# Kernel optimization log

Hardware: AMD Instinct MI355X
Metric: run time of the kernel (lower is better)

## Reference

```python
import jax, jax.numpy as jnp
import numpy as np

N, M, K, KD = 400000, 300000, 27, 8
CIN, C0, NCLS = 4, 32, 19
EPS = 1e-5


def setup_inputs() -> dict:
    key = jax.random.key(0)
    ks = jax.random.split(key, 20)
    point_fea = jax.random.normal(ks[0], (N, CIN), jnp.float32)
    idx_query = jax.random.randint(ks[1], (N,), 0, M, jnp.int32)
    nbrs = jax.random.randint(ks[2], (M, K), -1, M, jnp.int32)  # -1 = missing neighbor
    idx_dev = jax.random.randint(ks[3], (N, KD), -1, M, jnp.int32)
    w_raw = jax.random.uniform(ks[4], (N, KD), jnp.float32)
    w_dev = w_raw / jnp.sum(w_raw, axis=1, keepdims=True)  # trilinear weights sum to 1
    def w(k, *shape):
        fan = shape[-2] * K if len(shape) == 3 else shape[0]
        return jax.random.normal(k, shape, jnp.float32) / np.sqrt(fan)
    return {
        'point_fea': point_fea, 'idx_query': idx_query, 'nbrs': nbrs,
        'idx_dev': idx_dev, 'w_dev': w_dev,
        'W_s1': w(ks[5], K, CIN, C0), 'W_s2': w(ks[6], K, C0, C0),
        'g_s1': jnp.ones((C0,)), 'b_s1': jnp.zeros((C0,)),
        'g_s2': jnp.ones((C0,)), 'b_s2': jnp.zeros((C0,)),
        'W_r1': w(ks[7], K, C0, C0), 'W_r2': w(ks[8], K, C0, C0),
        'g_r1': jnp.ones((C0,)), 'b_r1': jnp.zeros((C0,)),
        'g_r2': jnp.ones((C0,)), 'b_r2': jnp.zeros((C0,)),
        'W_c': w(ks[9], C0, NCLS), 'b_c': jnp.zeros((NCLS,)),
    }


def sparse_conv(x, W, nbrs):
    # x: [M, Cin], W: [K, Cin, Cout], nbrs: [M, K] (-1 = miss)
    out = jnp.zeros((x.shape[0], W.shape[2]), x.dtype)
    for k in range(W.shape[0]):  # fixed small kernel-offset loop
        idx = nbrs[:, k]
        g = jnp.where((idx >= 0)[:, None], x[jnp.clip(idx, 0)], 0.0)
        out = out + g @ W[k]
    return out


def bn(x, g, b):
    m = jnp.mean(x, axis=0)
    v = jnp.var(x, axis=0)
    return (x - m) * jax.lax.rsqrt(v + EPS) * g + b


def reference(point_fea, idx_query, nbrs, idx_dev, w_dev,
              W_s1, W_s2, g_s1, b_s1, g_s2, b_s2,
              W_r1, W_r2, g_r1, b_r1, g_r2, b_r2, W_c, b_c):
    # spvoxelize: per-voxel mean of point features
    counts = jax.ops.segment_sum(jnp.ones((N,), jnp.float32), idx_query, M)
    vox = jax.ops.segment_sum(point_fea, idx_query, M) / jnp.maximum(counts, 1.0)[:, None]
    # stem: two sparse 3x3x3 convs + BN + ReLU
    h = jax.nn.relu(bn(sparse_conv(vox, W_s1, nbrs), g_s1, b_s1))
    h = jax.nn.relu(bn(sparse_conv(h, W_s2, nbrs), g_s2, b_s2))
    # ResidualBlock (inc == outc, stride 1 -> identity downsample)
    r = jax.nn.relu(bn(sparse_conv(h, W_r1, nbrs), g_r1, b_r1))
    r = bn(sparse_conv(r, W_r2, nbrs), g_r2, b_r2)
    h = jax.nn.relu(r + h)
    # spdevoxelize: masked trilinear 8-neighbor gather back to points
    g = jnp.where((idx_dev >= 0)[:, :, None], h[jnp.clip(idx_dev, 0)], 0.0)  # [N,8,C]
    pts = jnp.einsum('nkc,nk->nc', g, w_dev)
    # classifier
    return pts @ W_c + b_c
```

## Files before the change

kernel.cpp:

```cpp
#include <hip/hip_runtime.h>
#include <hip/hip_fp16.h>

#define NPTS 400000
#define MVOX 300000
#define KK 27
#define KD 8
#define CIN 4
#define C0 32
#define NCLS 19
#define EPS 1e-5f
#define NTILE (MVOX / 16)
#define GS1 ((MVOX + 255) / 256)
#define GT ((NTILE + 3) / 4)
#define NRED 64

typedef __attribute__((ext_vector_type(8))) _Float16 half8;
typedef __attribute__((ext_vector_type(4))) float f32x4;

__device__ __forceinline__ uint32_t pack2(float a, float b) {
    __half2 h = __floats2half2_rn(a, b);
    return __builtin_bit_cast(uint32_t, h);
}
__device__ __forceinline__ float2 unpack2(uint32_t u) {
    return __half22float2(__builtin_bit_cast(__half2, u));
}
__device__ __forceinline__ void unpack8(uint4 u, float* f) {
    float2 a = unpack2(u.x), b = unpack2(u.y), c = unpack2(u.z), d = unpack2(u.w);
    f[0] = a.x; f[1] = a.y; f[2] = b.x; f[3] = b.y;
    f[4] = c.x; f[5] = c.y; f[6] = d.x; f[7] = d.y;
}
__device__ __forceinline__ uint4 pack8(const float* f) {
    return make_uint4(pack2(f[0], f[1]), pack2(f[2], f[3]),
                      pack2(f[4], f[5]), pack2(f[6], f[7]));
}

__global__ void vox_accum(const float* __restrict__ pf, const int* __restrict__ iq,
                          float* __restrict__ counts, float* __restrict__ vox) {
    int i = blockIdx.x * blockDim.x + threadIdx.x;
    if (i >= NPTS) return;
    int q = iq[i];
    float4 f = *reinterpret_cast<const float4*>(pf + (size_t)i * CIN);
    atomicAdd(&counts[q], 1.0f);
    atomicAdd(&vox[q * CIN + 0], f.x);
    atomicAdd(&vox[q * CIN + 1], f.y);
    atomicAdd(&vox[q * CIN + 2], f.z);
    atomicAdd(&vox[q * CIN + 3], f.w);
}

__global__ void vox_div_h(const float4* __restrict__ vox, const float* __restrict__ counts,
                          uint2* __restrict__ voxh) {
    int i = blockIdx.x * blockDim.x + threadIdx.x;
    if (i >= MVOX) return;
    float inv = 1.0f / fmaxf(counts[i], 1.0f);
    float4 v = vox[i];
    voxh[i] = make_uint2(pack2(v.x * inv, v.y * inv), pack2(v.z * inv, v.w * inv));
}

__global__ void wprep(const float* __restrict__ W0, const float* __restrict__ W1,
                      const float* __restrict__ W2, uint4* __restrict__ Wf) {
    int t = blockIdx.x * blockDim.x + threadIdx.x;
    if (t >= 3 * KK * 128) return;
    int layer = t / (KK * 128);
    int rem = t % (KK * 128);
    int k = rem / 128;
    int h = (rem >> 6) & 1;
    int lane = rem & 63;
    const float* W = (layer == 0) ? W0 : (layer == 1) ? W1 : W2;
    const float* wk = W + k * (C0 * C0);
    int co = h * 16 + (lane & 15);
    int ci0 = (lane >> 4) * 8;
    float f[8];
#pragma unroll
    for (int j = 0; j < 8; j++) f[j] = wk[(ci0 + j) * C0 + co];
    Wf[t] = pack8(f);
}

__global__ __launch_bounds__(256) void conv_s1_h(const uint2* __restrict__ x,
                                                 const int* __restrict__ nbrs,
                                                 const float* __restrict__ W,
                                                 uint4* __restrict__ out,
                                                 float* __restrict__ partials) {
    int i = blockIdx.x * blockDim.x + threadIdx.x;
    const bool active = i < MVOX;
    float acc[C0];
#pragma unroll
    for (int c = 0; c < C0; c++) acc[c] = 0.f;
    if (active) {
        const int* nb = nbrs + (size_t)i * KK;
        int nbv[KK];
#pragma unroll
        for (int k = 0; k < KK; k++) nbv[k] = nb[k];
        uint2 pf[4];
#pragma unroll
        for (int k = 0; k < 4; k++) pf[k] = x[nbv[k] < 0 ? 0 : nbv[k]];
#pragma unroll
        for (int k = 0; k < KK; k++) {
            uint2 r = pf[k & 3];
            if (k + 4 < KK) pf[k & 3] = x[nbv[k + 4] < 0 ? 0 : nbv[k + 4]];
            float m = (nbv[k] >= 0) ? 1.f : 0.f;
            float2 ab = unpack2(r.x), cd = unpack2(r.y);
            float xs[4] = {m * ab.x, m * ab.y, m * cd.x, m * cd.y};
            const float* wk = W + k * (CIN * C0);
#pragma unroll
            for (int j = 0; j < 4; j++) {
#pragma unroll
                for (int co = 0; co < C0; co++) acc[co] += xs[j] * wk[j * C0 + co];
            }
        }
        uint4* o = out + (size_t)i * 4;
#pragma unroll
        for (int p = 0; p < 4; p++) o[p] = pack8(acc + p * 8);
    }
    float q[C0];
#pragma unroll
    for (int c = 0; c < C0; c++) q[c] = acc[c] * acc[c];
#pragma unroll
    for (int off = 32; off >= 1; off >>= 1) {
#pragma unroll
        for (int c = 0; c < C0; c++) {
            acc[c] += __shfl_down(acc[c], off);
            q[c] += __shfl_down(q[c], off);
        }
    }
    __shared__ float ls[4][64];
    const int wid = threadIdx.x >> 6, lane = threadIdx.x & 63;
    if (lane == 0) {
#pragma unroll
        for (int c = 0; c < C0; c++) { ls[wid][c] = acc[c]; ls[wid][C0 + c] = q[c]; }
    }
    __syncthreads();
    if (threadIdx.x < 64)
        partials[(size_t)blockIdx.x * 64 + threadIdx.x] =
            ls[0][threadIdx.x] + ls[1][threadIdx.x] + ls[2][threadIdx.x] + ls[3][threadIdx.x];
}

__global__ __launch_bounds__(256, 4) void conv32_mfma(const uint4* __restrict__ x,
                                                      const int* __restrict__ nbrs,
                                                      const uint4* __restrict__ Wf,
                                                      const float* __restrict__ ss,
                                                      __half* __restrict__ out,
                                                      float* __restrict__ partials) {
    const int lane = threadIdx.x & 63;
    const int wid = threadIdx.x >> 6;
    const int tile = blockIdx.x * 4 + wid;
    const bool active = tile < NTILE;
    const int row = lane & 15;
    const int chunk = lane >> 4;
    const int col = lane & 15;
    float sc[8], sh[8];
#pragma unroll
    for (int j = 0; j < 8; j++) {
        sc[j] = ss[chunk * 8 + j];
        sh[j] = ss[C0 + chunk * 8 + j];
    }
    f32x4 acc0 = {0.f, 0.f, 0.f, 0.f}, acc1 = {0.f, 0.f, 0.f, 0.f};
    if (active) {
        const int vr = tile * 16 + row;
        const int* nb = nbrs + (size_t)vr * KK;
        int nbv[KK];
#pragma unroll
        for (int k = 0; k < KK; k++) nbv[k] = nb[k];
        const uint4* xc = x + chunk;
        uint4 pf[8];
#pragma unroll
        for (int k = 0; k < 8; k++)
            pf[k] = xc[(size_t)(nbv[k] < 0 ? 0 : nbv[k]) * 4];
#pragma unroll
        for (int k = 0; k < KK; k++) {
            uint4 ar = pf[k & 7];
            if (k + 8 < KK)
                pf[k & 7] = xc[(size_t)(nbv[k + 8] < 0 ? 0 : nbv[k + 8]) * 4];
            float m = (nbv[k] >= 0) ? 1.f : 0.f;
            float f[8], g[8];
            unpack8(ar, f);
#pragma unroll
            for (int j = 0; j < 8; j++) g[j] = m * fmaxf(f[j] * sc[j] + sh[j], 0.f);
            half8 a = __builtin_bit_cast(half8, pack8(g));
            half8 b0 = __builtin_bit_cast(half8, Wf[k * 128 + lane]);
            half8 b1 = __builtin_bit_cast(half8, Wf[k * 128 + 64 + lane]);
            acc0 = __builtin_amdgcn_mfma_f32_16x16x32_f16(a, b0, acc0, 0, 0, 0);
            acc1 = __builtin_amdgcn_mfma_f32_16x16x32_f16(a, b1, acc1, 0, 0, 0);
        }
        __half* obase = out + (size_t)tile * 16 * C0;
#pragma unroll
        for (int r = 0; r < 4; r++) {
            int orow = chunk * 4 + r;
            obase[orow * C0 + col] = __float2half(acc0[r]);
            obase[orow * C0 + 16 + col] = __float2half(acc1[r]);
        }
    }
    float s0 = 0.f, q0 = 0.f, s1 = 0.f, q1 = 0.f;
#pragma unroll
    for (int r = 0; r < 4; r++) {
        s0 += acc0[r]; q0 += acc0[r] * acc0[r];
        s1 += acc1[r]; q1 += acc1[r] * acc1[r];
    }
    s0 += __shfl_xor(s0, 16); q0 += __shfl_xor(q0, 16);
    s1 += __shfl_xor(s1, 16); q1 += __shfl_xor(q1, 16);
    s0 += __shfl_xor(s0, 32); q0 += __shfl_xor(q0, 32);
    s1 += __shfl_xor(s1, 32); q1 += __shfl_xor(q1, 32);
    __shared__ float ls[4][64];
    if (lane < 16) {
        ls[wid][col] = s0;
        ls[wid][16 + col] = s1;
        ls[wid][32 + col] = q0;
        ls[wid][48 + col] = q1;
    }
    __syncthreads();
    if (threadIdx.x < 64)
        partials[(size_t)blockIdx.x * 64 + threadIdx.x] =
            ls[0][threadIdx.x] + ls[1][threadIdx.x] + ls[2][threadIdx.x] + ls[3][threadIdx.x];
}

__global__ __launch_bounds__(256) void bn_reduce(const float* __restrict__ partials,
                                                 int nblocks,
                                                 const float* __restrict__ g,
                                                 const float* __restrict__ b,
                                                 float* __restrict__ ss,
                                                 float* __restrict__ partial2,
                                                 unsigned int* __restrict__ cnt) {
    const int j = blockIdx.x;
    const int tid = threadIdx.x;
    const int c = tid & 63;
    const int sub = tid >> 6;
    const int per = (nblocks + NRED - 1) / NRED;
    int lo = j * per;
    int hi = lo + per; if (hi > nblocks) hi = nblocks;
    float acc = 0.f;
    for (int bk = lo + sub; bk < hi; bk += 4) acc += partials[(size_t)bk * 64 + c];
    __shared__ float ls[4][64];
    ls[sub][c] = acc;
    __syncthreads();
    if (tid < 64)
        partial2[(size_t)j * 64 + tid] = ls[0][tid] + ls[1][tid] + ls[2][tid] + ls[3][tid];
    __threadfence();
    __shared__ bool last;
    if (tid == 0) last = (atomicAdd(cnt, 1u) == NRED - 1);
    __syncthreads();
    if (!last) return;
    __threadfence();
    float a2 = 0.f;
    for (int bk = sub; bk < NRED; bk += 4) a2 += partial2[(size_t)bk * 64 + c];
    ls[sub][c] = a2;
    __syncthreads();
    if (tid < C0) {
        float s = ls[0][tid] + ls[1][tid] + ls[2][tid] + ls[3][tid];
        float q = ls[0][C0 + tid] + ls[1][C0 + tid] + ls[2][C0 + tid] + ls[3][C0 + tid];
        float mean = s * (1.0f / (float)MVOX);
        float var = q * (1.0f / (float)MVOX) - mean * mean;
        float scv = g[tid] * rsqrtf(var + EPS);
        ss[tid] = scv;
        ss[C0 + tid] = b[tid] - mean * scv;
    }
}

__global__ __launch_bounds__(256) void classify_pre(const uint4* __restrict__ D,
                                                    const uint4* __restrict__ B,
                                                    const float* __restrict__ ss_r2,
                                                    const float* __restrict__ ss_s2,
                                                    const float* __restrict__ Wc,
                                                    uint4* __restrict__ HC) {
    int v = blockIdx.x * blockDim.x + threadIdx.x;
    if (v >= MVOX) return;
    float f[C0], h[C0];
#pragma unroll
    for (int p = 0; p < 4; p++) {
        float tf[8], th[8];
        unpack8(D[(size_t)v * 4 + p], tf);
        unpack8(B[(size_t)v * 4 + p], th);
#pragma unroll
        for (int j = 0; j < 8; j++) { f[p * 8 + j] = tf[j]; h[p * 8 + j] = th[j]; }
    }
    float hh[C0];
#pragma unroll
    for (int j = 0; j < C0; j++) {
        float skip = fmaxf(h[j] * ss_s2[j] + ss_s2[C0 + j], 0.f);
        hh[j] = fmaxf(f[j] * ss_r2[j] + ss_r2[C0 + j] + skip, 0.f);
    }
    float o[24];
#pragma unroll
    for (int c = 0; c < 24; c++) o[c] = 0.f;
#pragma unroll
    for (int ci = 0; ci < C0; ci++) {
        float xv = hh[ci];
#pragma unroll
        for (int c = 0; c < NCLS; c++) o[c] += xv * Wc[ci * NCLS + c];
    }
    uint4* dst = HC + (size_t)v * 3;
    dst[0] = pack8(o);
    dst[1] = pack8(o + 8);
    dst[2] = pack8(o + 16);
}

__global__ __launch_bounds__(256) void devox_out(const uint4* __restrict__ HC,
                                                 const int4* __restrict__ idxd,
                                                 const float4* __restrict__ wdev,
                                                 const float* __restrict__ bc,
                                                 float* __restrict__ out) {
    int i = blockIdx.x * blockDim.x + threadIdx.x;
    if (i >= NPTS) return;
    int4 i0 = idxd[2 * i], i1 = idxd[2 * i + 1];
    float4 w0 = wdev[2 * i], w1 = wdev[2 * i + 1];
    int idxs[8] = {i0.x, i0.y, i0.z, i0.w, i1.x, i1.y, i1.z, i1.w};
    float wsv[8] = {w0.x, w0.y, w0.z, w0.w, w1.x, w1.y, w1.z, w1.w};
    float acc[24];
#pragma unroll
    for (int c = 0; c < 24; c++) acc[c] = 0.f;
    uint4 r[2][3];
    {
        const uint4* hr = HC + (size_t)(idxs[0] < 0 ? 0 : idxs[0]) * 3;
        r[0][0] = hr[0]; r[0][1] = hr[1]; r[0][2] = hr[2];
    }
#pragma unroll
    for (int k = 0; k < KD; k++) {
        int cur = k & 1;
        if (k + 1 < KD) {
            const uint4* hr = HC + (size_t)(idxs[k + 1] < 0 ? 0 : idxs[k + 1]) * 3;
            r[cur ^ 1][0] = hr[0]; r[cur ^ 1][1] = hr[1]; r[cur ^ 1][2] = hr[2];
        }
        float m = (idxs[k] >= 0) ? wsv[k] : 0.f;
#pragma unroll
        for (int p = 0; p < 3; p++) {
            float f[8]; unpack8(r[cur][p], f);
#pragma unroll
            for (int j = 0; j < 8; j++) acc[p * 8 + j] += m * f[j];
        }
    }
    float* op = out + (size_t)i * NCLS;
#pragma unroll
    for (int c = 0; c < NCLS; c++) op[c] = acc[c] + bc[c];
}

extern "C" void kernel_launch(void* const* d_in, const int* in_sizes, int n_in,
                              void* d_out, int out_size, void* d_ws, size_t ws_size,
                              hipStream_t stream) {
    const float* point_fea = (const float*)d_in[0];
    const int*   idx_query = (const int*)d_in[1];
    const int*   nbrs      = (const int*)d_in[2];
    const int*   idx_dev   = (const int*)d_in[3];
    const float* w_dev     = (const float*)d_in[4];
    const float* W_s1      = (const float*)d_in[5];
    const float* W_s2      = (const float*)d_in[6];
    const float* g_s1      = (const float*)d_in[7];
    const float* b_s1      = (const float*)d_in[8];
    const float* g_s2      = (const float*)d_in[9];
    const float* b_s2      = (const float*)d_in[10];
    const float* W_r1      = (const float*)d_in[11];
    const float* W_r2      = (const float*)d_in[12];
    const float* g_r1      = (const float*)d_in[13];
    const float* b_r1      = (const float*)d_in[14];
    const float* g_r2      = (const float*)d_in[15];
    const float* b_r2      = (const float*)d_in[16];
    const float* W_c       = (const float*)d_in[17];
    const float* b_c       = (const float*)d_in[18];
    float* out = (float*)d_out;

    float* ws = (float*)d_ws;
    const size_t M = MVOX;
    float* ss       = ws;
    float* partial2 = ws + 256;
    float* partials = partial2 + NRED * 64;
    unsigned int* cnt = (unsigned int*)(partials + (size_t)GT * 64);
    float* counts   = (float*)cnt + 64;
    float* vox32    = counts + M;
    uint2* voxh     = (uint2*)(vox32 + 4 * M);
    uint4* Wf       = (uint4*)((float*)voxh + 2 * M);
    float* bufs     = (float*)Wf + (size_t)3 * KK * 128 * 4;
    uint4* A = (uint4*)bufs;
    uint4* B = A + M * 4;
    uint4* C = B + M * 4;
    uint4* D = C + M * 4;

    hipMemsetAsync(cnt, 0, (size_t)(64 + 5 * M) * sizeof(float), stream);

    dim3 blk(256);
    dim3 gN((NPTS + 255) / 256);
    dim3 gM(GS1);
    dim3 gT(GT);
    dim3 gW((3 * KK * 128 + 255) / 256);

    vox_accum<<<gN, blk, 0, stream>>>(point_fea, idx_query, counts, vox32);
    vox_div_h<<<gM, blk, 0, stream>>>((const float4*)vox32, counts, voxh);
    wprep<<<gW, blk, 0, stream>>>(W_s2, W_r1, W_r2, Wf);

    conv_s1_h<<<gM, blk, 0, stream>>>(voxh, nbrs, W_s1, A, partials);
    bn_reduce<<<NRED, blk, 0, stream>>>(partials, GS1, g_s1, b_s1, ss + 0, partial2, cnt + 0);

    conv32_mfma<<<gT, blk, 0, stream>>>(A, nbrs, Wf + 0 * KK * 128, ss + 0, (__half*)B, partials);
    bn_reduce<<<NRED, blk, 0, stream>>>(partials, GT, g_s2, b_s2, ss + 64, partial2, cnt + 1);

    conv32_mfma<<<gT, blk, 0, stream>>>(B, nbrs, Wf + 1 * KK * 128, ss + 64, (__half*)C, partials);
    bn_reduce<<<NRED, blk, 0, stream>>>(partials, GT, g_r1, b_r1, ss + 128, partial2, cnt + 2);

    conv32_mfma<<<gT, blk, 0, stream>>>(C, nbrs, Wf + 2 * KK * 128, ss + 128, (__half*)D, partials);
    bn_reduce<<<NRED, blk, 0, stream>>>(partials, GT, g_r2, b_r2, ss + 192, partial2, cnt + 3);

    classify_pre<<<gM, blk, 0, stream>>>(D, B, ss + 192, ss + 64, W_c, A);

    devox_out<<<gN, blk, 0, stream>>>(A, (const int4*)idx_dev,
                                      (const float4*)w_dev, b_c, out);
}
```

Before: 722.5 us.

## Drop manual gather prefetch in convs, relax launch bounds, pad classifier rows to 64B

Removes the explicit neighbor-index preload and rotating register prefetch buffers in both conv kernels and loads each neighbor row inside the unrolled loop instead, leaving scheduling to the compiler. It also drops the min-blocks hint of 4 on conv32_mfma, and widens the per-voxel classifier output from 48 to 64 bytes so devox gathers hit aligned rows. The aim is lower register pressure and aligned gathers. The cost is possibly less memory-level parallelism in the gathers and more bytes written per voxel.

```diff
diff --git a/kernel.cpp b/kernel.cpp
--- a/kernel.cpp
+++ b/kernel.cpp
@@ -87,17 +87,11 @@
     for (int c = 0; c < C0; c++) acc[c] = 0.f;
     if (active) {
         const int* nb = nbrs + (size_t)i * KK;
-        int nbv[KK];
-#pragma unroll
-        for (int k = 0; k < KK; k++) nbv[k] = nb[k];
-        uint2 pf[4];
-#pragma unroll
-        for (int k = 0; k < 4; k++) pf[k] = x[nbv[k] < 0 ? 0 : nbv[k]];
 #pragma unroll
         for (int k = 0; k < KK; k++) {
-            uint2 r = pf[k & 3];
-            if (k + 4 < KK) pf[k & 3] = x[nbv[k + 4] < 0 ? 0 : nbv[k + 4]];
-            float m = (nbv[k] >= 0) ? 1.f : 0.f;
+            int idx = nb[k];
+            float m = (idx >= 0) ? 1.f : 0.f;
+            uint2 r = x[idx < 0 ? 0 : idx];
             float2 ab = unpack2(r.x), cd = unpack2(r.y);
             float xs[4] = {m * ab.x, m * ab.y, m * cd.x, m * cd.y};
             const float* wk = W + k * (CIN * C0);
@@ -134,12 +128,12 @@
             ls[0][threadIdx.x] + ls[1][threadIdx.x] + ls[2][threadIdx.x] + ls[3][threadIdx.x];
 }
 
-__global__ __launch_bounds__(256, 4) void conv32_mfma(const uint4* __restrict__ x,
-                                                      const int* __restrict__ nbrs,
-                                                      const uint4* __restrict__ Wf,
-                                                      const float* __restrict__ ss,
-                                                      __half* __restrict__ out,
-                                                      float* __restrict__ partials) {
+__global__ __launch_bounds__(256) void conv32_mfma(const uint4* __restrict__ x,
+                                                   const int* __restrict__ nbrs,
+                                                   const uint4* __restrict__ Wf,
+                                                   const float* __restrict__ ss,
+                                                   __half* __restrict__ out,
+                                                   float* __restrict__ partials) {
     const int lane = threadIdx.x & 63;
     const int wid = threadIdx.x >> 6;
     const int tile = blockIdx.x * 4 + wid;
@@ -157,20 +151,11 @@
     if (active) {
         const int vr = tile * 16 + row;
         const int* nb = nbrs + (size_t)vr * KK;
-        int nbv[KK];
-#pragma unroll
-        for (int k = 0; k < KK; k++) nbv[k] = nb[k];
-        const uint4* xc = x + chunk;
-        uint4 pf[8];
-#pragma unroll
-        for (int k = 0; k < 8; k++)
-            pf[k] = xc[(size_t)(nbv[k] < 0 ? 0 : nbv[k]) * 4];
 #pragma unroll
         for (int k = 0; k < KK; k++) {
-            uint4 ar = pf[k & 7];
-            if (k + 8 < KK)
-                pf[k & 7] = xc[(size_t)(nbv[k + 8] < 0 ? 0 : nbv[k + 8]) * 4];
-            float m = (nbv[k] >= 0) ? 1.f : 0.f;
+            int idx = nb[k];
+            float m = (idx >= 0) ? 1.f : 0.f;
+            uint4 ar = x[(size_t)(idx < 0 ? 0 : idx) * 4 + chunk];
             float f[8], g[8];
             unpack8(ar, f);
 #pragma unroll
@@ -277,19 +262,20 @@
         float skip = fmaxf(h[j] * ss_s2[j] + ss_s2[C0 + j], 0.f);
         hh[j] = fmaxf(f[j] * ss_r2[j] + ss_r2[C0 + j] + skip, 0.f);
     }
-    float o[24];
-#pragma unroll
-    for (int c = 0; c < 24; c++) o[c] = 0.f;
+    float o[32];
+#pragma unroll
+    for (int c = 0; c < 32; c++) o[c] = 0.f;
 #pragma unroll
     for (int ci = 0; ci < C0; ci++) {
         float xv = hh[ci];
 #pragma unroll
         for (int c = 0; c < NCLS; c++) o[c] += xv * Wc[ci * NCLS + c];
     }
-    uint4* dst = HC + (size_t)v * 3;
+    uint4* dst = HC + (size_t)v * 4;
     dst[0] = pack8(o);
     dst[1] = pack8(o + 8);
     dst[2] = pack8(o + 16);
+    dst[3] = pack8(o + 24);
 }
 
 __global__ __launch_bounds__(256) void devox_out(const uint4* __restrict__ HC,
@@ -308,14 +294,14 @@
     for (int c = 0; c < 24; c++) acc[c] = 0.f;
     uint4 r[2][3];
     {
-        const uint4* hr = HC + (size_t)(idxs[0] < 0 ? 0 : idxs[0]) * 3;
+        const uint4* hr = HC + (size_t)(idxs[0] < 0 ? 0 : idxs[0]) * 4;
         r[0][0] = hr[0]; r[0][1] = hr[1]; r[0][2] = hr[2];
     }
 #pragma unroll
     for (int k = 0; k < KD; k++) {
         int cur = k & 1;
         if (k + 1 < KD) {
-            const uint4* hr = HC + (size_t)(idxs[k + 1] < 0 ? 0 : idxs[k + 1]) * 3;
+            const uint4* hr = HC + (size_t)(idxs[k + 1] < 0 ? 0 : idxs[k + 1]) * 4;
             r[cur ^ 1][0] = hr[0]; r[cur ^ 1][1] = hr[1]; r[cur ^ 1][2] = hr[2];
         }
         float m = (idxs[k] >= 0) ? wsv[k] : 0.f;
```

New measurement: 764.2 us. 5.8% more time.
